# Kernel tuning notes

Measured on AMD Instinct MI355X. Metric: run time of the kernel, lower is better.

The kernel has to match this reference:

```python
import jax, jax.numpy as jnp
import numpy as np

# Dims from GlobalFractalRouterConfig defaults
B, D, FP, H, NF, A = 65536, 512, 64, 256, 4, 32


def _norm(x):
    # F.normalize(dim=-1) with eps=1e-12
    return x / jnp.clip(jnp.linalg.norm(x, axis=-1, keepdims=True), 1e-12)


def setup_inputs() -> dict:
    key = jax.random.key(0)
    ks = jax.random.split(key, 12)
    s = 0.02
    return {
        "features": jax.random.normal(ks[0], (B, D), jnp.float32),
        "source_fingerprint": jax.random.normal(ks[1], (FP,), jnp.float32),
        "target_fingerprint": jax.random.normal(ks[2], (FP,), jnp.float32),
        # field_generators: NF stacked (Linear(D+FP,H) -> GELU -> Linear(H,1))
        "Wf1": jax.random.normal(ks[3], (NF, D + FP, H), jnp.float32) * s,
        "bf1": jnp.zeros((NF, H), jnp.float32),
        "Wf2": jax.random.normal(ks[4], (NF, H), jnp.float32) * s,
        "bf2": jnp.zeros((NF,), jnp.float32),
        # compat_proj: Linear(2*FP, NF)
        "Wc": jax.random.normal(ks[5], (2 * FP, NF), jnp.float32) * s,
        "bc": jnp.zeros((NF,), jnp.float32),
        # gate_net: Linear(2*NF+FP, H) -> GELU -> Linear(H, D) -> Sigmoid
        "Wg1": jax.random.normal(ks[6], (2 * NF + FP, H), jnp.float32) * s,
        "bg1": jnp.zeros((H,), jnp.float32),
        "Wg2": jax.random.normal(ks[7], (H, D), jnp.float32) * s,
        "bg2": jnp.zeros((D,), jnp.float32),
        # AnchorBank
        "E": jax.random.normal(ks[8], (A, D), jnp.float32) * s,  # anchor_embeddings
        "Wfp": jax.random.normal(ks[9], (D, D), jnp.float32) * s,  # feature_proj
        "bfp": jnp.zeros((D,), jnp.float32),
        "Wfq": jax.random.normal(ks[10], (FP, D), jnp.float32) * s,  # fingerprint_proj
        "bfq": jnp.zeros((D,), jnp.float32),
    }


def _potential(feats, fp_vec, Wf1, bf1, Wf2, bf2):
    # AdjacentGate.compute_potential, all fields vectorized
    b = feats.shape[0]
    comb = jnp.concatenate(
        [feats, jnp.broadcast_to(fp_vec, (b, fp_vec.shape[0]))], axis=-1
    )  # [B, D+FP]
    h = jax.nn.gelu(jnp.einsum('bi,fih->bfh', comb, Wf1) + bf1, approximate=False)
    return jnp.einsum('bfh,fh->bf', h, Wf2) + bf2  # [B, NF]


def reference(features, source_fingerprint, target_fingerprint,
              Wf1, bf1, Wf2, bf2, Wc, bc, Wg1, bg1, Wg2, bg2,
              E, Wfp, bfp, Wfq, bfq):
    b = features.shape[0]
    # --- AdjacentGate ---
    p_src = _potential(features, source_fingerprint, Wf1, bf1, Wf2, bf2)
    p_tgt = _potential(features, target_fingerprint, Wf1, bf1, Wf2, bf2)
    gradient = p_tgt - p_src  # [B, NF]
    fp_comb = jnp.concatenate([source_fingerprint, target_fingerprint])  # [2*FP]
    compat = jnp.tanh(fp_comb @ Wc + bc)  # [NF]
    gate_in = jnp.concatenate(
        [gradient,
         jnp.broadcast_to(compat, (b, compat.shape[0])),
         jnp.broadcast_to(source_fingerprint, (b, source_fingerprint.shape[0]))],
        axis=-1)  # [B, 2*NF+FP]
    gate = jax.nn.sigmoid(
        jax.nn.gelu(gate_in @ Wg1 + bg1, approximate=False) @ Wg2 + bg2)  # [B, D]
    gated = features * gate
    # --- AnchorBank ---
    feat_proj = _norm(gated @ Wfp + bfp)  # [B, D]
    anchors_norm = _norm(E)  # [A, D]
    aff = feat_proj @ anchors_norm.T  # [B, A]
    fp_proj = source_fingerprint @ Wfq + bfq  # [D]
    aff = aff + 0.3 * (anchors_norm @ fp_proj)
    aff = jax.nn.softmax(aff, axis=-1)
    anchor_features = aff @ E  # [B, D]
    return gated + anchor_features
```

## Files before the change

### kernel.cpp

```cpp
#include <hip/hip_runtime.h>
#include <hip/hip_bf16.h>

typedef unsigned short u16;
typedef __attribute__((ext_vector_type(8))) __bf16 bf16x8;
typedef __attribute__((ext_vector_type(8))) short  s16x8;
typedef __attribute__((ext_vector_type(4))) short  s16x4;
typedef __attribute__((ext_vector_type(4))) float  f32x4;

#define NB 65536
#define OFF_GRAD   0u
#define OFF_SUMSQ  1048576u
#define OFF_CONSTS 1310720u
#define OFF_WF1T   1327104u
#define OFF_WG2T   2375680u
#define OFF_WFPT   2637824u
#define OFF_ET     3162112u
#define OFF_AFF    3194880u
#define OFF_GATED  7389184u
#define WS_NEEDED  74498048u
#define CI_SRC   0
#define CI_TGT   1024
#define CI_C0    2048
#define CI_INVE  2304
#define CI_ABIAS 2336

__device__ inline float bf2f(u16 u) { union { unsigned int i; float f; } v; v.i = ((unsigned int)u) << 16; return v.f; }
__device__ inline u16 f2bf(float f) { union { float f; unsigned int i; } v; v.f = f; return (u16)((v.i + 0x7fffu + ((v.i >> 16) & 1u)) >> 16); }
__device__ inline float gelu(float x) {
  float z = 1.5957691216f * x * (1.0f + 0.044715f * x * x);
  return x * __builtin_amdgcn_rcpf(1.0f + __expf(-z));
}
__device__ inline float sigm(float x) { return __builtin_amdgcn_rcpf(1.0f + __expf(-x)); }

__global__ __launch_bounds__(256) void k_pre(
    const float* __restrict__ sfp, const float* __restrict__ tfp,
    const float* __restrict__ wf1, const float* __restrict__ bf1,
    const float* __restrict__ wc,  const float* __restrict__ bc,
    const float* __restrict__ wg1, const float* __restrict__ bg1,
    const float* __restrict__ wfq, const float* __restrict__ bfq,
    const float* __restrict__ E,   float* __restrict__ consts)
{
  __shared__ float s_s[64], s_t[64], s_c[4], s_fp[512];
  const int t = threadIdx.x;
  const int b = blockIdx.x;
  if (t < 64) { s_s[t] = sfp[t]; s_t[t] = tfp[t]; }
  __syncthreads();
  if (b < 8) {
    if (t < 128) {
      int n = b * 128 + t;
      int f = n >> 8, h = n & 255;
      float as = bf1[f * 256 + h];
      float at = as;
      const float* col = wf1 + f * 147456 + 512 * 256 + h;
      #pragma unroll 8
      for (int j = 0; j < 64; ++j) {
        float wv = col[j * 256];
        as += s_s[j] * wv; at += s_t[j] * wv;
      }
      consts[CI_SRC + n] = as;
      consts[CI_TGT + n] = at;
    }
  } else if (b == 8) {
    if (t < 4) {
      float a = bc[t];
      for (int j = 0; j < 64; ++j)
        a += s_s[j] * wc[j * 4 + t] + s_t[j] * wc[(64 + j) * 4 + t];
      s_c[t] = tanhf(a);
    }
    __syncthreads();
    float a = bg1[t];
    #pragma unroll
    for (int f = 0; f < 4; ++f) a += s_c[f] * wg1[(4 + f) * 256 + t];
    for (int j = 0; j < 64; ++j) a += s_s[j] * wg1[(8 + j) * 256 + t];
    consts[CI_C0 + t] = a;
  } else {
    for (int d = t; d < 512; d += 256) {
      float a = bfq[d];
      for (int j = 0; j < 64; ++j) a += s_s[j] * wfq[j * 512 + d];
      s_fp[d] = a;
    }
    __syncthreads();
    if (t < 32) {
      float ss = 0.f, dot = 0.f;
      for (int d = 0; d < 512; ++d) {
        float e = E[t * 512 + d];
        ss += e * e; dot += e * s_fp[d];
      }
      float inv = 1.0f / fmaxf(sqrtf(ss), 1e-12f);
      consts[CI_INVE + t] = inv;
      consts[CI_ABIAS + t] = 0.3f * inv * dot;
    }
  }
}

__global__ __launch_bounds__(256) void k_transpose(
    const float* __restrict__ wf1, const float* __restrict__ wg2,
    const float* __restrict__ wfp, const float* __restrict__ E,
    u16* __restrict__ ws16)
{
  int tile = blockIdx.x;
  const float* src; u16* dst; int K, N, tl;
  if (tile < 512)      { int f = tile >> 7; tl = tile & 127; src = wf1 + f * 147456; dst = ws16 + (OFF_WF1T >> 1) + f * 131072; K = 512; N = 256; }
  else if (tile < 640) { tl = tile - 512; src = wg2; dst = ws16 + (OFF_WG2T >> 1); K = 256; N = 512; }
  else if (tile < 896) { tl = tile - 640; src = wfp; dst = ws16 + (OFF_WFPT >> 1); K = 512; N = 512; }
  else                 { tl = tile - 896; src = E;   dst = ws16 + (OFF_ET   >> 1); K = 32;  N = 512; }
  int ntn = N >> 5;
  int r0 = (tl / ntn) << 5, c0 = (tl % ntn) << 5;
  __shared__ float T[32][33];
  const int t = threadIdx.x;
  {
    int r = t >> 3, c4 = (t & 7) << 2;
    float4 v = *(const float4*)(src + (r0 + r) * N + c0 + c4);
    T[r][c4] = v.x; T[r][c4 + 1] = v.y; T[r][c4 + 2] = v.z; T[r][c4 + 3] = v.w;
  }
  __syncthreads();
  {
    int c = t >> 3, r4 = (t & 7) << 2;
    s16x4 v;
    v[0] = (short)f2bf(T[r4 + 0][c]); v[1] = (short)f2bf(T[r4 + 1][c]);
    v[2] = (short)f2bf(T[r4 + 2][c]); v[3] = (short)f2bf(T[r4 + 3][c]);
    *(s16x4*)(dst + (c0 + c) * K + r0 + r4) = v;
  }
}

__global__ __launch_bounds__(256, 2) void k_potential(
    const float* __restrict__ feat, const u16* __restrict__ wf1t,
    const float* __restrict__ wf2,  const float* __restrict__ consts,
    float* __restrict__ grad)
{
  __shared__ u16 Al[128][40];
  __shared__ u16 Bl[256][40];
  const int col0 = blockIdx.x << 8;
  const int row0 = blockIdx.y << 7;
  const int f = blockIdx.x;
  const int t = threadIdx.x;
  const int w = t >> 6, lane = t & 63, lr = lane & 15, lq = lane >> 4;

  f32x4 acc[2][16];
  #pragma unroll
  for (int i = 0; i < 2; ++i)
    #pragma unroll
    for (int j = 0; j < 16; ++j) { f32x4 z = {0.f, 0.f, 0.f, 0.f}; acc[i][j] = z; }

  for (int k0 = 0; k0 < 512; k0 += 32) {
    __syncthreads();
    #pragma unroll
    for (int i = 0; i < 4; ++i) {
      int s = t + (i << 8);
      int r = s >> 3, c4 = (s & 7) << 2;
      float4 v = *(const float4*)(feat + (row0 + r) * 512 + k0 + c4);
      s16x4 b;
      b[0] = (short)f2bf(v.x); b[1] = (short)f2bf(v.y);
      b[2] = (short)f2bf(v.z); b[3] = (short)f2bf(v.w);
      *(s16x4*)&Al[r][c4] = b;
    }
    #pragma unroll
    for (int i = 0; i < 4; ++i) {
      int s = t + (i << 8);
      int r = s >> 2, k8 = (s & 3) << 3;
      *(bf16x8*)&Bl[r][k8] = *(const bf16x8*)(wf1t + (col0 + r) * 512 + k0 + k8);
    }
    __syncthreads();
    bf16x8 a[2];
    #pragma unroll
    for (int rt = 0; rt < 2; ++rt)
      a[rt] = *(const bf16x8*)&Al[(w << 5) + (rt << 4) + lr][lq << 3];
    #pragma unroll
    for (int ct = 0; ct < 16; ++ct) {
      bf16x8 bb = *(const bf16x8*)&Bl[(ct << 4) + lr][lq << 3];
      acc[0][ct] = __builtin_amdgcn_mfma_f32_16x16x32_bf16(a[0], bb, acc[0][ct], 0, 0, 0);
      acc[1][ct] = __builtin_amdgcn_mfma_f32_16x16x32_bf16(a[1], bb, acc[1][ct], 0, 0, 0);
    }
  }
  float part[2][4] = {{0, 0, 0, 0}, {0, 0, 0, 0}};
  #pragma unroll
  for (int ct = 0; ct < 16; ++ct) {
    int n = col0 + (ct << 4) + lr;
    float so = consts[CI_SRC + n];
    float to = consts[CI_TGT + n];
    float w2 = wf2[n];
    #pragma unroll
    for (int rt = 0; rt < 2; ++rt)
      #pragma unroll
      for (int j = 0; j < 4; ++j) {
        float c = acc[rt][ct][j];
        part[rt][j] += (gelu(c + to) - gelu(c + so)) * w2;
      }
  }
  #pragma unroll
  for (int m = 1; m <= 8; m <<= 1)
    #pragma unroll
    for (int rt = 0; rt < 2; ++rt)
      #pragma unroll
      for (int j = 0; j < 4; ++j)
        part[rt][j] += __shfl_xor(part[rt][j], m, 64);
  if (lr == 0) {
    #pragma unroll
    for (int rt = 0; rt < 2; ++rt)
      #pragma unroll
      for (int j = 0; j < 4; ++j) {
        int r = row0 + (w << 5) + (rt << 4) + (lq << 2) + j;
        grad[r * 4 + f] = part[rt][j];
      }
  }
}

__global__ __launch_bounds__(256, 2) void k_gate(
    const float* __restrict__ feat, const float* __restrict__ grad,
    const float* __restrict__ wg1,  const u16* __restrict__ wg2t,
    const float* __restrict__ bg2,  const float* __restrict__ consts,
    u16* __restrict__ gated)
{
  __shared__ u16 Hl[128][264];
  __shared__ u16 Bl[128][40];
  const int col0 = blockIdx.x << 7;
  const int row0 = blockIdx.y << 7;
  const int t = threadIdx.x;
  const int w = t >> 6, lane = t & 63, lr = lane & 15, lq = lane >> 4;

  {
    float wv[4], c0v = consts[CI_C0 + t];
    #pragma unroll
    for (int f = 0; f < 4; ++f) wv[f] = wg1[f * 256 + t];
    for (int i = 0; i < 128; ++i) {
      float4 g = *(const float4*)(grad + ((row0 + i) << 2));
      float p = c0v + g.x * wv[0] + g.y * wv[1] + g.z * wv[2] + g.w * wv[3];
      Hl[i][t] = f2bf(gelu(p));
    }
  }
  f32x4 acc[2][8];
  #pragma unroll
  for (int i = 0; i < 2; ++i)
    #pragma unroll
    for (int j = 0; j < 8; ++j) { f32x4 z = {0.f, 0.f, 0.f, 0.f}; acc[i][j] = z; }

  for (int k0 = 0; k0 < 256; k0 += 32) {
    __syncthreads();
    #pragma unroll
    for (int i = 0; i < 2; ++i) {
      int s = t + (i << 8);
      int r = s >> 2, k8 = (s & 3) << 3;
      *(bf16x8*)&Bl[r][k8] = *(const bf16x8*)(wg2t + (col0 + r) * 256 + k0 + k8);
    }
    __syncthreads();
    bf16x8 a[2];
    #pragma unroll
    for (int rt = 0; rt < 2; ++rt)
      a[rt] = *(const bf16x8*)&Hl[(w << 5) + (rt << 4) + lr][k0 + (lq << 3)];
    #pragma unroll
    for (int ct = 0; ct < 8; ++ct) {
      bf16x8 bb = *(const bf16x8*)&Bl[(ct << 4) + lr][lq << 3];
      acc[0][ct] = __builtin_amdgcn_mfma_f32_16x16x32_bf16(a[0], bb, acc[0][ct], 0, 0, 0);
      acc[1][ct] = __builtin_amdgcn_mfma_f32_16x16x32_bf16(a[1], bb, acc[1][ct], 0, 0, 0);
    }
  }
  __syncthreads();
  u16* Gl = &Hl[0][0];
  #pragma unroll
  for (int ct = 0; ct < 8; ++ct) {
    int n = col0 + (ct << 4) + lr;
    float bv = bg2[n];
    #pragma unroll
    for (int rt = 0; rt < 2; ++rt)
      #pragma unroll
      for (int j = 0; j < 4; ++j) {
        int r = (w << 5) + (rt << 4) + (lq << 2) + j;
        Gl[r * 136 + (ct << 4) + lr] = f2bf(sigm(acc[rt][ct][j] + bv));
      }
  }
  __syncthreads();
  #pragma unroll
  for (int it = 0; it < 16; ++it) {
    int s = (it << 8) + t;
    int r = s >> 5, c4 = (s & 31) << 2;
    float4 f4 = *(const float4*)(feat + (row0 + r) * 512 + col0 + c4);
    s16x4 g4 = *(const s16x4*)(Gl + r * 136 + c4);
    s16x4 o;
    o[0] = (short)f2bf(f4.x * bf2f((u16)g4[0]));
    o[1] = (short)f2bf(f4.y * bf2f((u16)g4[1]));
    o[2] = (short)f2bf(f4.z * bf2f((u16)g4[2]));
    o[3] = (short)f2bf(f4.w * bf2f((u16)g4[3]));
    *(s16x4*)(gated + (row0 + r) * 512 + col0 + c4) = o;
  }
}

__global__ __launch_bounds__(256, 2) void k_proj(
    const u16* __restrict__ gated, const u16* __restrict__ wfpt,
    const float* __restrict__ bfp, u16* __restrict__ y,
    float* __restrict__ sumsq)
{
  __shared__ u16 U[128 * 264];
  u16 (*Al)[40] = (u16(*)[40])U;
  u16 (*Bl)[40] = (u16(*)[40])(U + 5120);
  const int col0 = blockIdx.x << 8;
  const int row0 = blockIdx.y << 7;
  const int t = threadIdx.x;
  const int w = t >> 6, lane = t & 63, lr = lane & 15, lq = lane >> 4;

  f32x4 acc[2][16];
  #pragma unroll
  for (int i = 0; i < 2; ++i)
    #pragma unroll
    for (int j = 0; j < 16; ++j) { f32x4 z = {0.f, 0.f, 0.f, 0.f}; acc[i][j] = z; }

  for (int k0 = 0; k0 < 512; k0 += 32) {
    __syncthreads();
    #pragma unroll
    for (int i = 0; i < 2; ++i) {
      int s = t + (i << 8);
      int r = s >> 2, k8 = (s & 3) << 3;
      *(bf16x8*)&Al[r][k8] = *(const bf16x8*)(gated + (row0 + r) * 512 + k0 + k8);
    }
    #pragma unroll
    for (int i = 0; i < 4; ++i) {
      int s = t + (i << 8);
      int r = s >> 2, k8 = (s & 3) << 3;
      *(bf16x8*)&Bl[r][k8] = *(const bf16x8*)(wfpt + (col0 + r) * 512 + k0 + k8);
    }
    __syncthreads();
    bf16x8 a[2];
    #pragma unroll
    for (int rt = 0; rt < 2; ++rt)
      a[rt] = *(const bf16x8*)&Al[(w << 5) + (rt << 4) + lr][lq << 3];
    #pragma unroll
    for (int ct = 0; ct < 16; ++ct) {
      bf16x8 bb = *(const bf16x8*)&Bl[(ct << 4) + lr][lq << 3];
      acc[0][ct] = __builtin_amdgcn_mfma_f32_16x16x32_bf16(a[0], bb, acc[0][ct], 0, 0, 0);
      acc[1][ct] = __builtin_amdgcn_mfma_f32_16x16x32_bf16(a[1], bb, acc[1][ct], 0, 0, 0);
    }
  }
  float part[2][4] = {{0, 0, 0, 0}, {0, 0, 0, 0}};
  #pragma unroll
  for (int ct = 0; ct < 16; ++ct) {
    float bv = bfp[col0 + (ct << 4) + lr];
    #pragma unroll
    for (int rt = 0; rt < 2; ++rt)
      #pragma unroll
      for (int j = 0; j < 4; ++j) {
        acc[rt][ct][j] += bv;
        part[rt][j] += acc[rt][ct][j] * acc[rt][ct][j];
      }
  }
  #pragma unroll
  for (int m = 1; m <= 8; m <<= 1)
    #pragma unroll
    for (int rt = 0; rt < 2; ++rt)
      #pragma unroll
      for (int j = 0; j < 4; ++j)
        part[rt][j] += __shfl_xor(part[rt][j], m, 64);
  if (lr == 0) {
    #pragma unroll
    for (int rt = 0; rt < 2; ++rt)
      #pragma unroll
      for (int j = 0; j < 4; ++j)
        atomicAdd(&sumsq[row0 + (w << 5) + (rt << 4) + (lq << 2) + j], part[rt][j]);
  }
  __syncthreads();
  u16* Yl = U;
  #pragma unroll
  for (int ct = 0; ct < 16; ++ct)
    #pragma unroll
    for (int rt = 0; rt < 2; ++rt)
      #pragma unroll
      for (int j = 0; j < 4; ++j) {
        int r = (w << 5) + (rt << 4) + (lq << 2) + j;
        Yl[r * 264 + (ct << 4) + lr] = f2bf(acc[rt][ct][j]);
      }
  __syncthreads();
  #pragma unroll
  for (int it = 0; it < 16; ++it) {
    int s = (it << 8) + t;
    int r = s >> 5, c8 = (s & 31) << 3;
    *(s16x8*)(y + (row0 + r) * 512 + col0 + c8) = *(const s16x8*)(Yl + r * 264 + c8);
  }
}

__global__ __launch_bounds__(256, 2) void k_aff(
    const u16* __restrict__ y, const float* __restrict__ E,
    const float* __restrict__ sumsq, const float* __restrict__ consts,
    u16* __restrict__ aff)
{
  __shared__ u16 El[32][520];
  __shared__ u16 Al[256][40];
  const int row0 = blockIdx.x << 8;
  const int t = threadIdx.x;
  const int w = t >> 6, lane = t & 63, lr = lane & 15, lq = lane >> 4;
  #pragma unroll
  for (int i = 0; i < 16; ++i) {
    int s = (i << 8) + t;
    int a = s >> 7, c4 = (s & 127) << 2;
    float4 v = *(const float4*)(E + a * 512 + c4);
    s16x4 b;
    b[0] = (short)f2bf(v.x); b[1] = (short)f2bf(v.y);
    b[2] = (short)f2bf(v.z); b[3] = (short)f2bf(v.w);
    *(s16x4*)&El[a][c4] = b;
  }
  f32x4 acc[4][2];
  #pragma unroll
  for (int i = 0; i < 4; ++i)
    #pragma unroll
    for (int j = 0; j < 2; ++j) { f32x4 z = {0.f, 0.f, 0.f, 0.f}; acc[i][j] = z; }

  for (int k0 = 0; k0 < 512; k0 += 32) {
    __syncthreads();
    #pragma unroll
    for (int i = 0; i < 4; ++i) {
      int s = (i << 8) + t;
      int r = s >> 2, k8 = (s & 3) << 3;
      *(bf16x8*)&Al[r][k8] = *(const bf16x8*)(y + (row0 + r) * 512 + k0 + k8);
    }
    __syncthreads();
    bf16x8 b0 = *(const bf16x8*)&El[lr][k0 + (lq << 3)];
    bf16x8 b1 = *(const bf16x8*)&El[16 + lr][k0 + (lq << 3)];
    #pragma unroll
    for (int rt = 0; rt < 4; ++rt) {
      bf16x8 a = *(const bf16x8*)&Al[(w << 6) + (rt << 4) + lr][lq << 3];
      acc[rt][0] = __builtin_amdgcn_mfma_f32_16x16x32_bf16(a, b0, acc[rt][0], 0, 0, 0);
      acc[rt][1] = __builtin_amdgcn_mfma_f32_16x16x32_bf16(a, b1, acc[rt][1], 0, 0, 0);
    }
  }
  float iv0 = consts[CI_INVE + lr],  iv1 = consts[CI_INVE + 16 + lr];
  float ab0 = consts[CI_ABIAS + lr], ab1 = consts[CI_ABIAS + 16 + lr];
  #pragma unroll
  for (int rt = 0; rt < 4; ++rt) {
    #pragma unroll
    for (int j = 0; j < 4; ++j) {
      int r = row0 + (w << 6) + (rt << 4) + (lq << 2) + j;
      float invn = 1.0f / fmaxf(sqrtf(sumsq[r]), 1e-12f);
      float v0 = acc[rt][0][j] * iv0 * invn + ab0;
      float v1 = acc[rt][1][j] * iv1 * invn + ab1;
      float mx = fmaxf(v0, v1);
      #pragma unroll
      for (int m = 1; m <= 8; m <<= 1) mx = fmaxf(mx, __shfl_xor(mx, m, 64));
      float e0 = __expf(v0 - mx), e1 = __expf(v1 - mx);
      float sm = e0 + e1;
      #pragma unroll
      for (int m = 1; m <= 8; m <<= 1) sm += __shfl_xor(sm, m, 64);
      float rs = 1.0f / sm;
      aff[r * 32 + lr]      = f2bf(e0 * rs);
      aff[r * 32 + 16 + lr] = f2bf(e1 * rs);
    }
  }
}

__global__ __launch_bounds__(256, 2) void k_out(
    const u16* __restrict__ gated, const u16* __restrict__ aff,
    const u16* __restrict__ et, float* __restrict__ out)
{
  __shared__ u16 ETl[512][40];
  __shared__ u16 Afl[64][40];
  __shared__ u16 Ol[64][520];
  const int row0 = blockIdx.x << 6;
  const int t = threadIdx.x;
  const int w = t >> 6, lane = t & 63, lr = lane & 15, lq = lane >> 4;
  {
    int r = t >> 2, k8 = (t & 3) << 3;
    *(bf16x8*)&Afl[r][k8] = *(const bf16x8*)(aff + (row0 + r) * 32 + k8);
  }
  #pragma unroll
  for (int i = 0; i < 8; ++i) {
    int s = (i << 8) + t;
    int d = s >> 2, k8 = (s & 3) << 3;
    *(bf16x8*)&ETl[d][k8] = *(const bf16x8*)(et + d * 32 + k8);
  }
  __syncthreads();
  bf16x8 a[4];
  #pragma unroll
  for (int rt = 0; rt < 4; ++rt)
    a[rt] = *(const bf16x8*)&Afl[(rt << 4) + lr][lq << 3];
  f32x4 z = {0.f, 0.f, 0.f, 0.f};
  #pragma unroll
  for (int ct = 0; ct < 8; ++ct) {
    bf16x8 bb = *(const bf16x8*)&ETl[(w << 7) + (ct << 4) + lr][lq << 3];
    #pragma unroll
    for (int rt = 0; rt < 4; ++rt) {
      f32x4 o = __builtin_amdgcn_mfma_f32_16x16x32_bf16(a[rt], bb, z, 0, 0, 0);
      #pragma unroll
      for (int j = 0; j < 4; ++j)
        Ol[(rt << 4) + (lq << 2) + j][(w << 7) + (ct << 4) + lr] = f2bf(o[j]);
    }
  }
  __syncthreads();
  #pragma unroll
  for (int it = 0; it < 32; ++it) {
    int s = (it << 8) + t;
    int r = s >> 7, c4 = (s & 127) << 2;
    s16x4 g4 = *(const s16x4*)(gated + (row0 + r) * 512 + c4);
    s16x4 a4 = *(const s16x4*)(&Ol[0][0] + r * 520 + c4);
    float4 o;
    o.x = bf2f((u16)g4[0]) + bf2f((u16)a4[0]);
    o.y = bf2f((u16)g4[1]) + bf2f((u16)a4[1]);
    o.z = bf2f((u16)g4[2]) + bf2f((u16)a4[2]);
    o.w = bf2f((u16)g4[3]) + bf2f((u16)a4[3]);
    *(float4*)(out + (row0 + r) * 512 + c4) = o;
  }
}

extern "C" void kernel_launch(void* const* d_in, const int* in_sizes, int n_in,
                              void* d_out, int out_size, void* d_ws, size_t ws_size,
                              hipStream_t stream) {
  (void)in_sizes; (void)n_in; (void)out_size;
  if (ws_size < WS_NEEDED) return;
  const float* feat = (const float*)d_in[0];
  const float* sfp  = (const float*)d_in[1];
  const float* tfp  = (const float*)d_in[2];
  const float* wf1  = (const float*)d_in[3];
  const float* bf1  = (const float*)d_in[4];
  const float* wf2  = (const float*)d_in[5];
  const float* wc   = (const float*)d_in[7];
  const float* bc   = (const float*)d_in[8];
  const float* wg1  = (const float*)d_in[9];
  const float* bg1  = (const float*)d_in[10];
  const float* wg2  = (const float*)d_in[11];
  const float* bg2  = (const float*)d_in[12];
  const float* E    = (const float*)d_in[13];
  const float* wfp  = (const float*)d_in[14];
  const float* bfp  = (const float*)d_in[15];
  const float* wfq  = (const float*)d_in[16];
  const float* bfq  = (const float*)d_in[17];

  char* ws = (char*)d_ws;
  float* grad   = (float*)(ws + OFF_GRAD);
  float* sumsq  = (float*)(ws + OFF_SUMSQ);
  float* consts = (float*)(ws + OFF_CONSTS);
  u16* ws16  = (u16*)ws;
  u16* wf1t  = (u16*)(ws + OFF_WF1T);
  u16* wg2t  = (u16*)(ws + OFF_WG2T);
  u16* wfpt  = (u16*)(ws + OFF_WFPT);
  u16* et    = (u16*)(ws + OFF_ET);
  u16* aff   = (u16*)(ws + OFF_AFF);
  u16* gated = (u16*)(ws + OFF_GATED);
  u16* yscr  = (u16*)d_out;
  float* out = (float*)d_out;

  hipMemsetAsync(ws + OFF_SUMSQ, 0, 262144, stream);
  k_pre<<<dim3(10), dim3(256), 0, stream>>>(sfp, tfp, wf1, bf1, wc, bc, wg1, bg1, wfq, bfq, E, consts);
  k_transpose<<<dim3(912), dim3(256), 0, stream>>>(wf1, wg2, wfp, E, ws16);
  k_potential<<<dim3(4, 512), dim3(256), 0, stream>>>(feat, wf1t, wf2, consts, grad);
  k_gate<<<dim3(4, 512), dim3(256), 0, stream>>>(feat, grad, wg1, wg2t, bg2, consts, gated);
  k_proj<<<dim3(2, 512), dim3(256), 0, stream>>>(gated, wfpt, bfp, yscr, sumsq);
  k_aff<<<dim3(256), dim3(256), 0, stream>>>(yscr, E, sumsq, consts, aff);
  k_out<<<dim3(1024), dim3(256), 0, stream>>>(gated, aff, et, out);
}
```

Measured before the change: 617.2 us.

## Pre-convert features to bf16 and stage GEMM tiles via direct global-to-LDS loads

Adds a conversion kernel that writes the fp32 features once as bf16 into spare space in the output buffer. k_potential and k_gate then read the bf16 copy instead of re-reading and converting fp32 features per column block. All GEMM A/B tile loads switch to global_load_lds with unpadded 32-wide LDS rows, which bypasses registers but may add LDS bank conflicts on the MFMA operand reads. The gating multiply now uses bf16-rounded features, which slightly changes numerics.

```diff
diff --git a/kernel.cpp b/kernel.cpp
--- a/kernel.cpp
+++ b/kernel.cpp
@@ -32,6 +32,24 @@
 }
 __device__ inline float sigm(float x) { return __builtin_amdgcn_rcpf(1.0f + __expf(-x)); }
 
+typedef __attribute__((address_space(3))) unsigned int as3_u32;
+typedef __attribute__((address_space(1))) unsigned int as1_u32;
+__device__ __forceinline__ void gload16(const u16* g, u16* l) {
+  __builtin_amdgcn_global_load_lds((const as1_u32*)g, (as3_u32*)l, 16, 0, 0);
+}
+
+__global__ __launch_bounds__(256) void k_cvt(const float* __restrict__ feat, u16* __restrict__ featbf) {
+  int idx = (blockIdx.x << 8) + threadIdx.x;
+  const float4* src = (const float4*)feat + (idx << 1);
+  float4 v0 = src[0], v1 = src[1];
+  s16x8 o;
+  o[0] = (short)f2bf(v0.x); o[1] = (short)f2bf(v0.y);
+  o[2] = (short)f2bf(v0.z); o[3] = (short)f2bf(v0.w);
+  o[4] = (short)f2bf(v1.x); o[5] = (short)f2bf(v1.y);
+  o[6] = (short)f2bf(v1.z); o[7] = (short)f2bf(v1.w);
+  *(s16x8*)(featbf + (idx << 3)) = o;
+}
+
 __global__ __launch_bounds__(256) void k_pre(
     const float* __restrict__ sfp, const float* __restrict__ tfp,
     const float* __restrict__ wf1, const float* __restrict__ bf1,
@@ -124,17 +142,18 @@
 }
 
 __global__ __launch_bounds__(256, 2) void k_potential(
-    const float* __restrict__ feat, const u16* __restrict__ wf1t,
+    const u16* __restrict__ featbf, const u16* __restrict__ wf1t,
     const float* __restrict__ wf2,  const float* __restrict__ consts,
     float* __restrict__ grad)
 {
-  __shared__ u16 Al[128][40];
-  __shared__ u16 Bl[256][40];
+  __shared__ u16 Al[128][32];
+  __shared__ u16 Bl[256][32];
   const int col0 = blockIdx.x << 8;
   const int row0 = blockIdx.y << 7;
   const int f = blockIdx.x;
   const int t = threadIdx.x;
   const int w = t >> 6, lane = t & 63, lr = lane & 15, lq = lane >> 4;
+  const int gr = lane >> 2, gc = (lane & 3) << 3;
 
   f32x4 acc[2][16];
   #pragma unroll
@@ -145,20 +164,14 @@
   for (int k0 = 0; k0 < 512; k0 += 32) {
     __syncthreads();
     #pragma unroll
-    for (int i = 0; i < 4; ++i) {
-      int s = t + (i << 8);
-      int r = s >> 3, c4 = (s & 7) << 2;
-      float4 v = *(const float4*)(feat + (row0 + r) * 512 + k0 + c4);
-      s16x4 b;
-      b[0] = (short)f2bf(v.x); b[1] = (short)f2bf(v.y);
-      b[2] = (short)f2bf(v.z); b[3] = (short)f2bf(v.w);
-      *(s16x4*)&Al[r][c4] = b;
-    }
-    #pragma unroll
-    for (int i = 0; i < 4; ++i) {
-      int s = t + (i << 8);
-      int r = s >> 2, k8 = (s & 3) << 3;
-      *(bf16x8*)&Bl[r][k8] = *(const bf16x8*)(wf1t + (col0 + r) * 512 + k0 + k8);
+    for (int j = 0; j < 2; ++j) {
+      int rb = (j << 6) + (w << 4);
+      gload16(featbf + (row0 + rb + gr) * 512 + k0 + gc, &Al[rb][0]);
+    }
+    #pragma unroll
+    for (int j = 0; j < 4; ++j) {
+      int rb = (j << 6) + (w << 4);
+      gload16(wf1t + (col0 + rb + gr) * 512 + k0 + gc, &Bl[rb][0]);
     }
     __syncthreads();
     bf16x8 a[2];
@@ -206,17 +219,18 @@
 }
 
 __global__ __launch_bounds__(256, 2) void k_gate(
-    const float* __restrict__ feat, const float* __restrict__ grad,
+    const u16* __restrict__ featbf, const float* __restrict__ grad,
     const float* __restrict__ wg1,  const u16* __restrict__ wg2t,
     const float* __restrict__ bg2,  const float* __restrict__ consts,
     u16* __restrict__ gated)
 {
   __shared__ u16 Hl[128][264];
-  __shared__ u16 Bl[128][40];
+  __shared__ u16 Bl[128][32];
   const int col0 = blockIdx.x << 7;
   const int row0 = blockIdx.y << 7;
   const int t = threadIdx.x;
   const int w = t >> 6, lane = t & 63, lr = lane & 15, lq = lane >> 4;
+  const int gr = lane >> 2, gc = (lane & 3) << 3;
 
   {
     float wv[4], c0v = consts[CI_C0 + t];
@@ -237,10 +251,9 @@
   for (int k0 = 0; k0 < 256; k0 += 32) {
     __syncthreads();
     #pragma unroll
-    for (int i = 0; i < 2; ++i) {
-      int s = t + (i << 8);
-      int r = s >> 2, k8 = (s & 3) << 3;
-      *(bf16x8*)&Bl[r][k8] = *(const bf16x8*)(wg2t + (col0 + r) * 256 + k0 + k8);
+    for (int j = 0; j < 2; ++j) {
+      int rb = (j << 6) + (w << 4);
+      gload16(wg2t + (col0 + rb + gr) * 256 + k0 + gc, &Bl[rb][0]);
     }
     __syncthreads();
     bf16x8 a[2];
@@ -270,17 +283,16 @@
   }
   __syncthreads();
   #pragma unroll
-  for (int it = 0; it < 16; ++it) {
+  for (int it = 0; it < 8; ++it) {
     int s = (it << 8) + t;
-    int r = s >> 5, c4 = (s & 31) << 2;
-    float4 f4 = *(const float4*)(feat + (row0 + r) * 512 + col0 + c4);
-    s16x4 g4 = *(const s16x4*)(Gl + r * 136 + c4);
-    s16x4 o;
-    o[0] = (short)f2bf(f4.x * bf2f((u16)g4[0]));
-    o[1] = (short)f2bf(f4.y * bf2f((u16)g4[1]));
-    o[2] = (short)f2bf(f4.z * bf2f((u16)g4[2]));
-    o[3] = (short)f2bf(f4.w * bf2f((u16)g4[3]));
-    *(s16x4*)(gated + (row0 + r) * 512 + col0 + c4) = o;
+    int r = s >> 4, c8 = (s & 15) << 3;
+    s16x8 f8 = *(const s16x8*)(featbf + (row0 + r) * 512 + col0 + c8);
+    s16x8 g8 = *(const s16x8*)(Gl + r * 136 + c8);
+    s16x8 o;
+    #pragma unroll
+    for (int j = 0; j < 8; ++j)
+      o[j] = (short)f2bf(bf2f((u16)f8[j]) * bf2f((u16)g8[j]));
+    *(s16x8*)(gated + (row0 + r) * 512 + col0 + c8) = o;
   }
 }
 
@@ -290,12 +302,13 @@
     float* __restrict__ sumsq)
 {
   __shared__ u16 U[128 * 264];
-  u16 (*Al)[40] = (u16(*)[40])U;
-  u16 (*Bl)[40] = (u16(*)[40])(U + 5120);
+  u16 (*Al)[32] = (u16(*)[32])U;
+  u16 (*Bl)[32] = (u16(*)[32])(U + 4096);
   const int col0 = blockIdx.x << 8;
   const int row0 = blockIdx.y << 7;
   const int t = threadIdx.x;
   const int w = t >> 6, lane = t & 63, lr = lane & 15, lq = lane >> 4;
+  const int gr = lane >> 2, gc = (lane & 3) << 3;
 
   f32x4 acc[2][16];
   #pragma unroll
@@ -306,16 +319,14 @@
   for (int k0 = 0; k0 < 512; k0 += 32) {
     __syncthreads();
     #pragma unroll
-    for (int i = 0; i < 2; ++i) {
-      int s = t + (i << 8);
-      int r = s >> 2, k8 = (s & 3) << 3;
-      *(bf16x8*)&Al[r][k8] = *(const bf16x8*)(gated + (row0 + r) * 512 + k0 + k8);
-    }
-    #pragma unroll
-    for (int i = 0; i < 4; ++i) {
-      int s = t + (i << 8);
-      int r = s >> 2, k8 = (s & 3) << 3;
-      *(bf16x8*)&Bl[r][k8] = *(const bf16x8*)(wfpt + (col0 + r) * 512 + k0 + k8);
+    for (int j = 0; j < 2; ++j) {
+      int rb = (j << 6) + (w << 4);
+      gload16(gated + (row0 + rb + gr) * 512 + k0 + gc, &Al[rb][0]);
+    }
+    #pragma unroll
+    for (int j = 0; j < 4; ++j) {
+      int rb = (j << 6) + (w << 4);
+      gload16(wfpt + (col0 + rb + gr) * 512 + k0 + gc, &Bl[rb][0]);
     }
     __syncthreads();
     bf16x8 a[2];
@@ -381,10 +392,11 @@
     u16* __restrict__ aff)
 {
   __shared__ u16 El[32][520];
-  __shared__ u16 Al[256][40];
+  __shared__ u16 Al[256][32];
   const int row0 = blockIdx.x << 8;
   const int t = threadIdx.x;
   const int w = t >> 6, lane = t & 63, lr = lane & 15, lq = lane >> 4;
+  const int gr = lane >> 2, gc = (lane & 3) << 3;
   #pragma unroll
   for (int i = 0; i < 16; ++i) {
     int s = (i << 8) + t;
@@ -404,10 +416,9 @@
   for (int k0 = 0; k0 < 512; k0 += 32) {
     __syncthreads();
     #pragma unroll
-    for (int i = 0; i < 4; ++i) {
-      int s = (i << 8) + t;
-      int r = s >> 2, k8 = (s & 3) << 3;
-      *(bf16x8*)&Al[r][k8] = *(const bf16x8*)(y + (row0 + r) * 512 + k0 + k8);
+    for (int j = 0; j < 4; ++j) {
+      int rb = (j << 6) + (w << 4);
+      gload16(y + (row0 + rb + gr) * 512 + k0 + gc, &Al[rb][0]);
     }
     __syncthreads();
     bf16x8 b0 = *(const bf16x8*)&El[lr][k0 + (lq << 3)];
@@ -531,13 +542,15 @@
   u16* aff   = (u16*)(ws + OFF_AFF);
   u16* gated = (u16*)(ws + OFF_GATED);
   u16* yscr  = (u16*)d_out;
+  u16* featbf = (u16*)d_out + 33554432;
   float* out = (float*)d_out;
 
   hipMemsetAsync(ws + OFF_SUMSQ, 0, 262144, stream);
+  k_cvt<<<dim3(16384), dim3(256), 0, stream>>>(feat, featbf);
   k_pre<<<dim3(10), dim3(256), 0, stream>>>(sfp, tfp, wf1, bf1, wc, bc, wg1, bg1, wfq, bfq, E, consts);
   k_transpose<<<dim3(912), dim3(256), 0, stream>>>(wf1, wg2, wfp, E, ws16);
-  k_potential<<<dim3(4, 512), dim3(256), 0, stream>>>(feat, wf1t, wf2, consts, grad);
-  k_gate<<<dim3(4, 512), dim3(256), 0, stream>>>(feat, grad, wg1, wg2t, bg2, consts, gated);
+  k_potential<<<dim3(4, 512), dim3(256), 0, stream>>>(featbf, wf1t, wf2, consts, grad);
+  k_gate<<<dim3(4, 512), dim3(256), 0, stream>>>(featbf, grad, wg1, wg2t, bg2, consts, gated);
   k_proj<<<dim3(2, 512), dim3(256), 0, stream>>>(gated, wfpt, bfp, yscr, sumsq);
   k_aff<<<dim3(256), dim3(256), 0, stream>>>(yscr, E, sumsq, consts, aff);
   k_out<<<dim3(1024), dim3(256), 0, stream>>>(gated, aff, et, out);
```

Result: slower. 645.6 us (+4.6%).
